# Optimization experiments

Measured on AMD Instinct MI355X. Metric: run time of the kernel, lower is better.

Reference implementation:

```python
import jax, jax.numpy as jnp
import numpy as np

B, CIN, COUT, H, W = 8, 256, 256, 64, 64


def setup_inputs() -> dict:
    key = jax.random.key(0)
    k1, k2, k3 = jax.random.split(key, 3)
    x = jax.random.normal(k1, (B, CIN, H, W), dtype=jnp.float32)
    style = jax.random.normal(k2, (B, CIN), dtype=jnp.float32)
    # kaiming_normal_ (fan_in = CIN*3*3, gain = sqrt(2))
    fan_in = CIN * 9
    weight = jax.random.normal(k3, (COUT, CIN, 3, 3), dtype=jnp.float32) * np.sqrt(2.0 / fan_in)
    return {"x": x, "style": style, "weight": weight}


def reference(x, style, weight):
    b, cin, h, w = x.shape
    cout = weight.shape[0]
    # modulate: [B, Cout, Cin, 3, 3]
    mw = style[:, None, :, None, None] * weight[None]
    # demodulate
    sigma = jnp.sqrt(jnp.sum(mw * mw, axis=(2, 3, 4), keepdims=True) + 1e-8)
    dw = mw / sigma
    # per-sample conv via grouped convolution (groups = B)
    x_g = x.reshape(1, b * cin, h, w)
    w_g = dw.reshape(b * cout, cin, 3, 3)
    out = jax.lax.conv_general_dilated(
        x_g, w_g,
        window_strides=(1, 1),
        padding=((1, 1), (1, 1)),
        feature_group_count=b,
        dimension_numbers=("NCHW", "OIHW", "NCHW"),
    )
    return out.reshape(b, cout, h, w)
```

## Files before the change

kernel.cpp:

```cpp
#include <hip/hip_runtime.h>

#define B_ 8
#define CIN_ 256
#define COUT_ 256

typedef short short8_t __attribute__((ext_vector_type(8)));
typedef float float4_t __attribute__((ext_vector_type(4)));

#define DWA_SHORTS   (B_ * 9 * 32 * COUT_ * 8)
#define XPRE_SHORTS  (B_ * 8 * 66 * 66 * 32)

__device__ __forceinline__ unsigned short f2bf(float f) {
    union { float f; unsigned u; } v; v.f = f;
    unsigned u = v.u;
    unsigned r = (u + 0x7fffu + ((u >> 16) & 1u)) >> 16;
    return (unsigned short)r;
}

__device__ __forceinline__ void gload_lds16(const unsigned short* g, unsigned short* l) {
    __builtin_amdgcn_global_load_lds(
        (__attribute__((address_space(1))) void*)(g),
        (__attribute__((address_space(3))) void*)(l), 16, 0, 0);
}

__global__ __launch_bounds__(256) void k_prep(const float* __restrict__ x,
                                              const float* __restrict__ style,
                                              const float* __restrict__ weight,
                                              unsigned short* __restrict__ xpre,
                                              unsigned short* __restrict__ dwA) {
    __shared__ float wlds[4 * 2304];
    const int blk = blockIdx.x;
    const int t = threadIdx.x;

    if (blk >= 64) {
        const int e = blk - 64;
        const int hp = e % 33;
        const int q2 = e / 33;
        const int cb = q2 & 7, b = q2 >> 3;
        const float* xslab = x + ((size_t)(b * CIN_ + cb * 32)) * 4096;
        unsigned short* dst_slab = xpre + ((size_t)(b * 8 + cb) * 66) * 2112;

#pragma unroll
        for (int rr = 0; rr < 2; ++rr) {
            const int h_out = hp * 2 + rr;
            const int h_in = h_out - 1;
            unsigned short* dst_row = dst_slab + (size_t)h_out * 2112;
#pragma unroll
            for (int pass = 0; pass < 2; ++pass) {
                int p = t + pass * 256;
                if (p >= 264) break;
                int w_out = p >> 2, g = p & 3;
                int w_in = w_out - 1;
                short8_t v = (short8_t){0, 0, 0, 0, 0, 0, 0, 0};
                if ((unsigned)h_in < 64u && (unsigned)w_in < 64u) {
                    const float* xp = xslab + ((size_t)(g * 8) * 64 + h_in) * 64 + w_in;
#pragma unroll
                    for (int j = 0; j < 8; ++j) v[j] = (short)f2bf(xp[(size_t)j * 4096]);
                }
                const int chunk = g ^ ((w_out >> 1) & 3);
                *(short8_t*)(dst_row + (size_t)w_out * 32 + chunk * 8) = v;
            }
        }
        return;
    }

    const int co_l = t >> 6;
    const int lane = t & 63;
    const int co = blk * 4 + co_l;

    const float* wp = weight + (size_t)(blk * 4) * 2304;
#pragma unroll
    for (int k = 0; k < 36; ++k) wlds[t + 256 * k] = wp[t + 256 * k];
    __syncthreads();

    float wv[4][9];
    float ss[4];
#pragma unroll
    for (int k = 0; k < 4; ++k) {
        float a = 0.f;
#pragma unroll
        for (int tap = 0; tap < 9; ++tap) {
            float w = wlds[co_l * 2304 + (lane + 64 * k) * 9 + tap];
            wv[k][tap] = w;
            a += w * w;
        }
        ss[k] = a;
    }
    float sv[8][4];
#pragma unroll
    for (int b = 0; b < 8; ++b)
#pragma unroll
        for (int k = 0; k < 4; ++k) sv[b][k] = style[b * CIN_ + lane + 64 * k];

    float inv[8];
#pragma unroll
    for (int b = 0; b < 8; ++b) {
        float part = 0.f;
#pragma unroll
        for (int k = 0; k < 4; ++k) part += sv[b][k] * sv[b][k] * ss[k];
#pragma unroll
        for (int off = 32; off > 0; off >>= 1) part += __shfl_xor(part, off, 64);
        inv[b] = 1.0f / sqrtf(part + 1e-8f);
    }

    const size_t base = (size_t)co * 8 + (lane & 7) + (size_t)(lane >> 3) * 2048;
#pragma unroll
    for (int b = 0; b < 8; ++b)
#pragma unroll
        for (int tap = 0; tap < 9; ++tap)
#pragma unroll
            for (int k = 0; k < 4; ++k) {
                size_t addr = ((size_t)(b * 9 + tap) * 32 + k * 8) * 2048 + base;
                dwA[addr] = f2bf(wv[k][tap] * sv[b][k] * inv[b]);
            }
}

__global__ __launch_bounds__(256, 2) void k_conv(const unsigned short* __restrict__ xpre,
                                                 const unsigned short* __restrict__ dwA,
                                                 float* __restrict__ out) {
    __shared__ __align__(16) unsigned short xs[2][4 * 66 * 32];

    const int b = blockIdx.x;
    const int co_tile = blockIdx.y;
    const int rowgrp = blockIdx.z;
    const int tid = threadIdx.x;
    const int lane = tid & 63, wid = tid >> 6;
    const int wave_m = wid >> 1, wave_n = wid & 1;
    const int quad = lane >> 4, l16 = lane & 15;
    const int r0 = rowgrp * 2;
    const int co_base = co_tile * 128 + wave_m * 64;

    float4_t acc[4][4];
#pragma unroll
    for (int mi = 0; mi < 4; ++mi)
#pragma unroll
        for (int ni = 0; ni < 4; ++ni) acc[mi][ni] = (float4_t){0.f, 0.f, 0.f, 0.f};

    const unsigned short* src_base = xpre + (size_t)b * 8 * 66 * 66 * 32;

    auto stage = [&](int cb, int buf) {
        const unsigned short* s = src_base + ((size_t)cb * 66 + r0) * 2112;
        unsigned short* d = xs[buf];
#pragma unroll
        for (int k = 0; k < 4; ++k)
            gload_lds16(s + (size_t)(tid + k * 256) * 8, d + (size_t)(tid + k * 256) * 8);
        if (tid < 32)
            gload_lds16(s + (size_t)(tid + 1024) * 8, d + (size_t)(tid + 1024) * 8);
    };

    short8_t abuf[3][4];
    auto loadA = [&](short8_t* dst, int acb, int atap) {
        const unsigned short* Ab = dwA + ((size_t)(b * 9 + atap) * 32 + acb * 4 + quad) * 2048
                                       + (size_t)(co_base + l16) * 8;
#pragma unroll
        for (int mi = 0; mi < 4; ++mi)
            dst[mi] = *(const short8_t*)(Ab + mi * 128);
    };

    short8_t bf[2][4];
    auto readB = [&](short8_t* dst, const unsigned short* xb, int tap) {
        const int dh = tap / 3, dwc = tap % 3;
        const unsigned short* brow = xb + (wave_n + dh) * (66 * 32);
#pragma unroll
        for (int ni = 0; ni < 4; ++ni) {
            const int col = ni * 16 + l16 + dwc;
            dst[ni] = *(const short8_t*)(brow + col * 32 + (quad ^ ((col >> 1) & 3)) * 8);
        }
    };

    stage(0, 0);
    loadA(abuf[0], 0, 0);
    loadA(abuf[1], 0, 1);

    for (int cb = 0; cb < 8; ++cb) {
        __syncthreads();
        if (cb < 7) stage(cb + 1, (cb + 1) & 1);

        const unsigned short* xb = xs[cb & 1];
        readB(bf[0], xb, 0);
#pragma unroll
        for (int tap = 0; tap < 9; ++tap) {
            const int nl = tap + 2;
            const int acb = cb + nl / 9, atap = nl % 9;
            if (acb < 8) loadA(abuf[nl % 3], acb, atap);
            if (tap < 8) readB(bf[(tap + 1) & 1], xb, tap + 1);

            const short8_t* ac = abuf[tap % 3];
            const short8_t* bc = bf[tap & 1];
            __builtin_amdgcn_s_setprio(1);
#pragma unroll
            for (int mi = 0; mi < 4; ++mi)
#pragma unroll
                for (int ni = 0; ni < 4; ++ni)
                    acc[mi][ni] = __builtin_amdgcn_mfma_f32_16x16x32_bf16(
                        ac[mi], bc[ni], acc[mi][ni], 0, 0, 0);
            __builtin_amdgcn_s_setprio(0);
        }
    }

    const int orow = r0 + wave_n;
#pragma unroll
    for (int mi = 0; mi < 4; ++mi)
#pragma unroll
        for (int ni = 0; ni < 4; ++ni)
#pragma unroll
            for (int r = 0; r < 4; ++r) {
                int co = co_base + mi * 16 + quad * 4 + r;
                int c = ni * 16 + l16;
                out[(((size_t)b * COUT_ + co) * 64 + (size_t)orow) * 64 + c] = acc[mi][ni][r];
            }
}

extern "C" void kernel_launch(void* const* d_in, const int* in_sizes, int n_in,
                              void* d_out, int out_size, void* d_ws, size_t ws_size,
                              hipStream_t stream) {
    const float* x = (const float*)d_in[0];
    const float* style = (const float*)d_in[1];
    const float* weight = (const float*)d_in[2];
    float* out = (float*)d_out;

    unsigned short* dwA = (unsigned short*)d_ws;
    unsigned short* xpre = dwA + DWA_SHORTS;

    k_prep<<<dim3(64 + B_ * 8 * 33), 256, 0, stream>>>(x, style, weight, xpre, dwA);
    k_conv<<<dim3(8, 2, 32), 256, 0, stream>>>(xpre, dwA, out);
}
```

Measured before the change: 125.4 us.

## Load conv input fragments directly from global memory instead of LDS staging

Removes the LDS double buffer and the per-channel-block __syncthreads, and has each wave load its B operand fragments straight from global memory into registers. The fragments use the same three-deep register prefetch pipeline as the weights. The aim is to drop the barrier and LDS traffic and to free LDS for occupancy. The cost is redundant global and L2 reads, since the overlapping 3x3 taps and the waves sharing rows now each fetch their own copies.

```diff
diff --git a/kernel.cpp b/kernel.cpp
--- a/kernel.cpp
+++ b/kernel.cpp
@@ -15,12 +15,6 @@
     unsigned u = v.u;
     unsigned r = (u + 0x7fffu + ((u >> 16) & 1u)) >> 16;
     return (unsigned short)r;
-}
-
-__device__ __forceinline__ void gload_lds16(const unsigned short* g, unsigned short* l) {
-    __builtin_amdgcn_global_load_lds(
-        (__attribute__((address_space(1))) void*)(g),
-        (__attribute__((address_space(3))) void*)(l), 16, 0, 0);
 }
 
 __global__ __launch_bounds__(256) void k_prep(const float* __restrict__ x,
@@ -118,8 +112,6 @@
 __global__ __launch_bounds__(256, 2) void k_conv(const unsigned short* __restrict__ xpre,
                                                  const unsigned short* __restrict__ dwA,
                                                  float* __restrict__ out) {
-    __shared__ __align__(16) unsigned short xs[2][4 * 66 * 32];
-
     const int b = blockIdx.x;
     const int co_tile = blockIdx.y;
     const int rowgrp = blockIdx.z;
@@ -138,16 +130,6 @@
 
     const unsigned short* src_base = xpre + (size_t)b * 8 * 66 * 66 * 32;
 
-    auto stage = [&](int cb, int buf) {
-        const unsigned short* s = src_base + ((size_t)cb * 66 + r0) * 2112;
-        unsigned short* d = xs[buf];
-#pragma unroll
-        for (int k = 0; k < 4; ++k)
-            gload_lds16(s + (size_t)(tid + k * 256) * 8, d + (size_t)(tid + k * 256) * 8);
-        if (tid < 32)
-            gload_lds16(s + (size_t)(tid + 1024) * 8, d + (size_t)(tid + 1024) * 8);
-    };
-
     short8_t abuf[3][4];
     auto loadA = [&](short8_t* dst, int acb, int atap) {
         const unsigned short* Ab = dwA + ((size_t)(b * 9 + atap) * 32 + acb * 4 + quad) * 2048
@@ -157,10 +139,10 @@
             dst[mi] = *(const short8_t*)(Ab + mi * 128);
     };
 
-    short8_t bf[2][4];
-    auto readB = [&](short8_t* dst, const unsigned short* xb, int tap) {
-        const int dh = tap / 3, dwc = tap % 3;
-        const unsigned short* brow = xb + (wave_n + dh) * (66 * 32);
+    short8_t bbuf[3][4];
+    auto loadB = [&](short8_t* dst, int acb, int atap) {
+        const int dh = atap / 3, dwc = atap % 3;
+        const unsigned short* brow = src_base + ((size_t)acb * 66 + r0 + wave_n + dh) * 2112;
 #pragma unroll
         for (int ni = 0; ni < 4; ++ni) {
             const int col = ni * 16 + l16 + dwc;
@@ -168,25 +150,22 @@
         }
     };
 
-    stage(0, 0);
     loadA(abuf[0], 0, 0);
+    loadB(bbuf[0], 0, 0);
     loadA(abuf[1], 0, 1);
+    loadB(bbuf[1], 0, 1);
 
     for (int cb = 0; cb < 8; ++cb) {
-        __syncthreads();
-        if (cb < 7) stage(cb + 1, (cb + 1) & 1);
-
-        const unsigned short* xb = xs[cb & 1];
-        readB(bf[0], xb, 0);
 #pragma unroll
         for (int tap = 0; tap < 9; ++tap) {
             const int nl = tap + 2;
             const int acb = cb + nl / 9, atap = nl % 9;
-            if (acb < 8) loadA(abuf[nl % 3], acb, atap);
-            if (tap < 8) readB(bf[(tap + 1) & 1], xb, tap + 1);
-
+            if (acb < 8) {
+                loadA(abuf[nl % 3], acb, atap);
+                loadB(bbuf[nl % 3], acb, atap);
+            }
             const short8_t* ac = abuf[tap % 3];
-            const short8_t* bc = bf[tap & 1];
+            const short8_t* bc = bbuf[tap % 3];
             __builtin_amdgcn_s_setprio(1);
 #pragma unroll
             for (int mi = 0; mi < 4; ++mi)
```

Result: slower. 134.4 us (+7.2%).
